# Kernel optimization log

Hardware: AMD Instinct MI355X
Metric: run time of the kernel (lower is better)

The kernel has to match this reference:

```python
import jax, jax.numpy as jnp
import numpy as np

B, NP, NFFT, SPACING = 4096, 512, 4096, 8


def setup_inputs() -> dict:
    key = jax.random.key(0)
    LS_ri = jax.random.normal(key, (B, NP, 2), dtype=jnp.float32)  # real/imag of LS_est
    # 1-based comb pilot positions: 1, 9, ..., 4089 (sorted, min == 1)
    pilot_pos = 1.0 + SPACING * jnp.arange(NP, dtype=jnp.float32)
    # nn.Parameter init: log(exp(initial_decay) - 1), initial_decay = 0.5
    decay_param = jnp.array([np.log(np.exp(0.5) - 1.0)], dtype=jnp.float32)
    return {"LS_ri": LS_ri, "pilot_pos": pilot_pos, "decay_param": decay_param, "Nfft": NFFT}


def reference(LS_ri, pilot_pos, decay_param, Nfft):
    # decay = softplus(raw param)
    decay = jax.nn.softplus(decay_param[0])
    # torch code: if min(pilot_loc) == 1 -> shift to 0-based (true by construction)
    loc = pilot_pos - 1.0                                  # [NP], 0-based pilot locations
    H = LS_ri                                              # [B, NP, 2]

    # pilot_loc[0] > 0 branch: linearly extrapolate a pilot at subcarrier 0
    slope_l = (H[:, 1] - H[:, 0]) / (loc[1] - loc[0])      # [B, 2]
    h0 = H[:, 0] - slope_l * loc[0]
    # pilot_loc[-1] < Nfft-1 branch: extrapolate a pilot at subcarrier Nfft-1
    slope_r = (H[:, -1] - H[:, -2]) / (loc[-1] - loc[-2])
    hN = H[:, -1] + slope_r * (Nfft - 1 - loc[-1])

    H = jnp.concatenate([h0[:, None], H, hN[:, None]], axis=1)           # [B, NP+2, 2]
    loc = jnp.concatenate([jnp.zeros((1,), loc.dtype), loc,
                           jnp.full((1,), Nfft - 1, loc.dtype)])          # [NP+2]

    i = jnp.arange(Nfft, dtype=loc.dtype)                                 # [Nfft]
    left = jnp.clip(jnp.searchsorted(loc, i, side='right') - 1, 0, loc.shape[0] - 2)
    right = left + 1
    x0, x1 = loc[left], loc[right]                                        # [Nfft]
    y0, y1 = H[:, left], H[:, right]                                      # [B, Nfft, 2]

    w_l = jnp.exp(-decay * jnp.abs(i - x0))                               # [Nfft]
    w_r = jnp.exp(-decay * jnp.abs(x1 - i))
    w = (w_l + w_r + 1e-12)
    out = (w_l[None, :, None] * y0 + w_r[None, :, None] * y1) / w[None, :, None]
    return out  # [B, Nfft, 2] (real/imag of complex estimate)
```

## Files before the change

kernel.cpp:

```cpp
#include <hip/hip_runtime.h>


#define NP_C    512
#define NFFT_C  4096
#define ROWS_C  4
#define THREADS 256

__global__ void dai_weights_kernel(const float* __restrict__ pilot_pos,
                                   const float* __restrict__ decay_param,
                                   float4* __restrict__ wout,
                                   int NP, int Nfft) {
    int i = blockIdx.x * blockDim.x + threadIdx.x;
    if (i >= Nfft) return;

    float decay = log1pf(expf(decay_param[0]));
    float fi = (float)i;

    int lo = 0, hi = NP;
    while (lo < hi) {
        int mid = (lo + hi) >> 1;
        if (pilot_pos[mid] - 1.0f <= fi) lo = mid + 1; else hi = mid;
    }
    int count = 1 + lo + (((float)(Nfft - 1)) <= fi ? 1 : 0);
    int left = min(max(count - 1, 0), NP);
    int right = left + 1;

    float x0 = (left == 0) ? 0.0f
             : (left <= NP ? pilot_pos[left - 1] - 1.0f : (float)(Nfft - 1));
    float x1 = (right <= NP) ? pilot_pos[right - 1] - 1.0f : (float)(Nfft - 1);

    float wl = expf(-decay * fabsf(fi - x0));
    float wr = expf(-decay * fabsf(x1 - fi));
    float w = wl + wr + 1e-12f;

    float4 o;
    o.x = wl / w;
    o.y = wr / w;
    o.z = __int_as_float(left);
    o.w = 0.0f;
    wout[i] = o;
}

__global__ __launch_bounds__(THREADS) void dai_interp_mr(
        const float* __restrict__ LS,
        const float* __restrict__ pilot_pos,
        const float4* __restrict__ wts,
        float* __restrict__ out) {
    constexpr int NP = NP_C, NFFT = NFFT_C, ROWS = ROWS_C;
    constexpr int PAIRS = NFFT / 2;
    constexpr int PPT = PAIRS / THREADS;

    __shared__ float2 hext[2][NP + 2];

    const int t = threadIdx.x;
    const int b0 = blockIdx.x * ROWS;

    float4 w0[PPT], w1[PPT];
#pragma unroll
    for (int j = 0; j < PPT; ++j) {
        int p = t + THREADS * j;
        w0[j] = wts[2 * p];
        w1[j] = wts[2 * p + 1];
    }

    const float loc0  = pilot_pos[0] - 1.0f;
    const float loc1  = pilot_pos[1] - 1.0f;
    const float locll = pilot_pos[NP - 2] - 1.0f;
    const float locl  = pilot_pos[NP - 1] - 1.0f;
    const float inv_l = 1.0f / (loc1 - loc0);
    const float inv_r = 1.0f / (locl - locll);
    const float tr    = (float)(NFFT - 1) - locl;

    auto stage = [&](int r, int buf) {
        const float* rowp = LS + (size_t)(b0 + r) * NP * 2;
        float4 v = ((const float4*)rowp)[t];
        float2* dst = hext[buf];
        dst[1 + 2 * t] = make_float2(v.x, v.y);
        dst[2 + 2 * t] = make_float2(v.z, v.w);
        if (t == 0) {
            float2 H0  = ((const float2*)rowp)[0];
            float2 H1  = ((const float2*)rowp)[1];
            float2 Hll = ((const float2*)rowp)[NP - 2];
            float2 Hl  = ((const float2*)rowp)[NP - 1];
            float2 h0, hN;
            h0.x = H0.x - (H1.x - H0.x) * inv_l * loc0;
            h0.y = H0.y - (H1.y - H0.y) * inv_l * loc0;
            hN.x = Hl.x + (Hl.x - Hll.x) * inv_r * tr;
            hN.y = Hl.y + (Hl.y - Hll.y) * inv_r * tr;
            dst[0] = h0;
            dst[NP + 1] = hN;
        }
    };

    stage(0, 0);
    __syncthreads();

    for (int r = 0; r < ROWS; ++r) {
        if (r + 1 < ROWS) stage(r + 1, (r + 1) & 1);

        const float2* h = hext[r & 1];
        float4* out4 = (float4*)(out + (size_t)(b0 + r) * NFFT * 2);
#pragma unroll
        for (int j = 0; j < PPT; ++j) {
            int p = t + THREADS * j;
            int l0 = __float_as_int(w0[j].z);
            int l1 = __float_as_int(w1[j].z);
            float2 y00 = h[l0], y01 = h[l0 + 1];
            float2 y10 = h[l1], y11 = h[l1 + 1];
            float4 o;
            o.x = w0[j].x * y00.x + w0[j].y * y01.x;
            o.y = w0[j].x * y00.y + w0[j].y * y01.y;
            o.z = w1[j].x * y10.x + w1[j].y * y11.x;
            o.w = w1[j].x * y10.y + w1[j].y * y11.y;
            out4[p] = o;
        }
        __syncthreads();
    }
}

__global__ __launch_bounds__(256) void dai_interp_generic(
        const float* __restrict__ LS, const float* __restrict__ pilot_pos,
        const float4* __restrict__ wts, float* __restrict__ out,
        int NP, int Nfft) {
    extern __shared__ float2 hext[];
    const int b = blockIdx.x;
    const int t = threadIdx.x;
    {
        const float2* row2 = (const float2*)(LS + (size_t)b * NP * 2);
        for (int idx = t; idx < NP; idx += 256) hext[1 + idx] = row2[idx];
    }
    __syncthreads();
    if (t == 0) {
        float2 H0 = hext[1], H1 = hext[2];
        float2 Hl = hext[NP], Hll = hext[NP - 1];
        float loc0 = pilot_pos[0] - 1.0f, loc1 = pilot_pos[1] - 1.0f;
        float locl = pilot_pos[NP - 1] - 1.0f, locll = pilot_pos[NP - 2] - 1.0f;
        float sl = 1.0f / (loc1 - loc0), sr = 1.0f / (locl - locll);
        float trr = (float)(Nfft - 1) - locl;
        hext[0] = make_float2(H0.x - (H1.x - H0.x) * sl * loc0,
                              H0.y - (H1.y - H0.y) * sl * loc0);
        hext[NP + 1] = make_float2(Hl.x + (Hl.x - Hll.x) * sr * trr,
                                   Hl.y + (Hl.y - Hll.y) * sr * trr);
    }
    __syncthreads();
    float2* out2 = (float2*)(out + (size_t)b * Nfft * 2);
    for (int i = t; i < Nfft; i += 256) {
        float4 w = wts[i];
        int l = __float_as_int(w.z);
        float2 y0 = hext[l], y1 = hext[l + 1];
        out2[i] = make_float2(w.x * y0.x + w.y * y1.x,
                              w.x * y0.y + w.y * y1.y);
    }
}

extern "C" void kernel_launch(void* const* d_in, const int* in_sizes, int n_in,
                              void* d_out, int out_size, void* d_ws, size_t ws_size,
                              hipStream_t stream) {
    const float* LS     = (const float*)d_in[0];
    const float* pilot  = (const float*)d_in[1];
    const float* decayp = (const float*)d_in[2];

    const int NP   = in_sizes[1];
    const int B    = in_sizes[0] / (2 * NP);
    const int Nfft = out_size / (2 * B);

    float4* wts = (float4*)d_ws;

    dai_weights_kernel<<<(Nfft + 255) / 256, 256, 0, stream>>>(
        pilot, decayp, wts, NP, Nfft);

    if (NP == NP_C && Nfft == NFFT_C && (B % ROWS_C) == 0) {
        dai_interp_mr<<<B / ROWS_C, THREADS, 0, stream>>>(
            LS, pilot, wts, (float*)d_out);
    } else {
        dai_interp_generic<<<B, 256, (NP + 2) * sizeof(float2), stream>>>(
            LS, pilot, wts, (float*)d_out, NP, Nfft);
    }
}
```

Before: 156.5 us.

## Gather pilots directly from global/L1 and use nontemporal output stores

Removes the shared-memory double-buffered staging of each pilot row and its barriers. Each thread now gathers the neighbouring pilots straight from global memory, relying on L1/L2 caching, and substitutes the extrapolated edge values with selects. Output writes use nontemporal stores to avoid polluting the cache with the large streaming output. The trade-off is more global load instructions per output and some redundant edge-value computation in every thread.

After: 188.3 us. 20.3% more time.

```diff
diff --git a/kernel.cpp b/kernel.cpp
--- a/kernel.cpp
+++ b/kernel.cpp
@@ -5,6 +5,8 @@
 #define NFFT_C  4096
 #define ROWS_C  4
 #define THREADS 256
+
+typedef float vf4 __attribute__((ext_vector_type(4)));
 
 __global__ void dai_weights_kernel(const float* __restrict__ pilot_pos,
                                    const float* __restrict__ decay_param,
@@ -41,7 +43,7 @@
     wout[i] = o;
 }
 
-__global__ __launch_bounds__(THREADS) void dai_interp_mr(
+__global__ __launch_bounds__(THREADS) void dai_interp_v4(
         const float* __restrict__ LS,
         const float* __restrict__ pilot_pos,
         const float4* __restrict__ wts,
@@ -49,8 +51,6 @@
     constexpr int NP = NP_C, NFFT = NFFT_C, ROWS = ROWS_C;
     constexpr int PAIRS = NFFT / 2;
     constexpr int PPT = PAIRS / THREADS;
-
-    __shared__ float2 hext[2][NP + 2];
 
     const int t = threadIdx.x;
     const int b0 = blockIdx.x * ROWS;
@@ -71,50 +71,41 @@
     const float inv_r = 1.0f / (locl - locll);
     const float tr    = (float)(NFFT - 1) - locl;
 
-    auto stage = [&](int r, int buf) {
-        const float* rowp = LS + (size_t)(b0 + r) * NP * 2;
-        float4 v = ((const float4*)rowp)[t];
-        float2* dst = hext[buf];
-        dst[1 + 2 * t] = make_float2(v.x, v.y);
-        dst[2 + 2 * t] = make_float2(v.z, v.w);
-        if (t == 0) {
-            float2 H0  = ((const float2*)rowp)[0];
-            float2 H1  = ((const float2*)rowp)[1];
-            float2 Hll = ((const float2*)rowp)[NP - 2];
-            float2 Hl  = ((const float2*)rowp)[NP - 1];
-            float2 h0, hN;
-            h0.x = H0.x - (H1.x - H0.x) * inv_l * loc0;
-            h0.y = H0.y - (H1.y - H0.y) * inv_l * loc0;
-            hN.x = Hl.x + (Hl.x - Hll.x) * inv_r * tr;
-            hN.y = Hl.y + (Hl.y - Hll.y) * inv_r * tr;
-            dst[0] = h0;
-            dst[NP + 1] = hN;
-        }
-    };
+    for (int r = 0; r < ROWS; ++r) {
+        const float2* __restrict__ row2 =
+            (const float2*)(LS + (size_t)(b0 + r) * NP * 2);
 
-    stage(0, 0);
-    __syncthreads();
+        float2 H0 = row2[0], H1 = row2[1];
+        float2 Hll = row2[NP - 2], Hl = row2[NP - 1];
+        float2 h0, hN;
+        h0.x = H0.x - (H1.x - H0.x) * inv_l * loc0;
+        h0.y = H0.y - (H1.y - H0.y) * inv_l * loc0;
+        hN.x = Hl.x + (Hl.x - Hll.x) * inv_r * tr;
+        hN.y = Hl.y + (Hl.y - Hll.y) * inv_r * tr;
 
-    for (int r = 0; r < ROWS; ++r) {
-        if (r + 1 < ROWS) stage(r + 1, (r + 1) & 1);
-
-        const float2* h = hext[r & 1];
-        float4* out4 = (float4*)(out + (size_t)(b0 + r) * NFFT * 2);
+        vf4* out4 = (vf4*)(out + (size_t)(b0 + r) * NFFT * 2);
 #pragma unroll
         for (int j = 0; j < PPT; ++j) {
             int p = t + THREADS * j;
             int l0 = __float_as_int(w0[j].z);
             int l1 = __float_as_int(w1[j].z);
-            float2 y00 = h[l0], y01 = h[l0 + 1];
-            float2 y10 = h[l1], y11 = h[l1 + 1];
-            float4 o;
+
+            float2 t00 = row2[max(l0 - 1, 0)];
+            float2 t01 = row2[min(l0, NP - 1)];
+            float2 t10 = row2[max(l1 - 1, 0)];
+            float2 t11 = row2[min(l1, NP - 1)];
+            float2 y00 = (l0 == 0)  ? h0 : t00;
+            float2 y01 = (l0 == NP) ? hN : t01;
+            float2 y10 = (l1 == 0)  ? h0 : t10;
+            float2 y11 = (l1 == NP) ? hN : t11;
+
+            vf4 o;
             o.x = w0[j].x * y00.x + w0[j].y * y01.x;
             o.y = w0[j].x * y00.y + w0[j].y * y01.y;
             o.z = w1[j].x * y10.x + w1[j].y * y11.x;
             o.w = w1[j].x * y10.y + w1[j].y * y11.y;
-            out4[p] = o;
+            __builtin_nontemporal_store(o, &out4[p]);
         }
-        __syncthreads();
     }
 }
 
@@ -170,7 +161,7 @@
         pilot, decayp, wts, NP, Nfft);
 
     if (NP == NP_C && Nfft == NFFT_C && (B % ROWS_C) == 0) {
-        dai_interp_mr<<<B / ROWS_C, THREADS, 0, stream>>>(
+        dai_interp_v4<<<B / ROWS_C, THREADS, 0, stream>>>(
             LS, pilot, wts, (float*)d_out);
     } else {
         dai_interp_generic<<<B, 256, (NP + 2) * sizeof(float2), stream>>>(
```
